# Kernel tuning notes

Hardware: AMD Instinct MI355X
Metric: run time of the kernel (lower is better)

## Reference

```python
import jax, jax.numpy as jnp
import numpy as np

D_MODEL = 1024
NUM_HEADS = 16
D_HEAD = D_MODEL // NUM_HEADS


def setup_inputs() -> dict:
    key = jax.random.key(0)
    ks = jax.random.split(key, 9)
    s = 1.0 / np.sqrt(D_MODEL)
    inp = {"x": jax.random.normal(ks[0], (2, 2048, D_MODEL), dtype=jnp.float32)}
    for i, name in enumerate(["q", "k", "v", "o"]):
        inp[f"W_{name}"] = jax.random.uniform(ks[1 + 2 * i], (D_MODEL, D_MODEL), minval=-s, maxval=s, dtype=jnp.float32)
        inp[f"b_{name}"] = jax.random.uniform(ks[2 + 2 * i], (D_MODEL,), minval=-s, maxval=s, dtype=jnp.float32)
    return inp


def reference(x, W_q, b_q, W_k, b_k, W_v, b_v, W_o, b_o):
    B, S, _ = x.shape
    def heads(W, b):
        # [B,S,D] @ [D,D] -> [B,S,H,Dh] -> [B,H,S,Dh]
        return (x @ W.T + b).reshape(B, S, NUM_HEADS, D_HEAD).transpose(0, 2, 1, 3)
    Q, K, V = heads(W_q, b_q), heads(W_k, b_k), heads(W_v, b_v)
    scores = jnp.einsum("bhqd,bhkd->bhqk", Q, K) / jnp.sqrt(jnp.float32(D_HEAD))
    causal = jnp.tril(jnp.ones((S, S), dtype=bool))  # True = keep
    scores = jnp.where(causal, scores, -jnp.inf)
    A = jax.nn.softmax(scores, axis=-1)
    out = jnp.einsum("bhqk,bhkd->bhqd", A, V)  # [B,H,S,Dh]
    out = out.transpose(0, 2, 1, 3).reshape(B, S, D_MODEL)
    return out @ W_o.T + b_o
```

## Files before the change

### kernel.cpp

```cpp
#include <hip/hip_runtime.h>
#include <math.h>

#define D_MODEL 1024
#define NUM_HEADS 16
#define D_HEAD 64
#define SEQ 2048
#define BATCH 2
#define NROWS (BATCH * SEQ)

typedef short s8v __attribute__((ext_vector_type(8)));
typedef float f4v __attribute__((ext_vector_type(4)));

__device__ __forceinline__ short to_bf(float f) {
    union { float f; unsigned u; } x; x.f = f;
    unsigned r = x.u + 0x7fffu + ((x.u >> 16) & 1u);
    return (short)(r >> 16);
}

__device__ __forceinline__ unsigned pack_bf2(float a, float b) {
    return (unsigned)(unsigned short)to_bf(a) | ((unsigned)(unsigned short)to_bf(b) << 16);
}

__device__ __forceinline__ float fast_exp2(float x) {
    return __builtin_amdgcn_exp2f(x);
}

__device__ __forceinline__ void gld_lds16(const short* g, short* l) {
    __builtin_amdgcn_global_load_lds(
        (const __attribute__((address_space(1))) unsigned*)g,
        (__attribute__((address_space(3))) unsigned*)l, 16, 0, 0);
}

#define QSCALE 0.180336880f

__global__ __launch_bounds__(256) void cvt_fused(
    const float* __restrict__ x,  const float* __restrict__ Wq,
    const float* __restrict__ Wk, const float* __restrict__ Wv,
    const float* __restrict__ Wo,
    short* __restrict__ Xb, short* __restrict__ Wqkvb, short* __restrict__ Wob)
{
    const int NX = NROWS * D_MODEL / 4;
    const int NW = D_MODEL * D_MODEL / 4;
    int j = blockIdx.x * 256 + threadIdx.x;
    const float* src; short* dst; float sc = 1.f;
    if (j < NX)                 { src = x;  dst = Xb; }
    else if ((j -= NX) < NW)    { src = Wq; dst = Wqkvb; sc = QSCALE; }
    else if ((j -= NW) < NW)    { src = Wk; dst = Wqkvb + NW * 4; }
    else if ((j -= NW) < NW)    { src = Wv; dst = Wqkvb + NW * 8; }
    else                        { j -= NW; src = Wo; dst = Wob; }
    float4 v = ((const float4*)src)[j];
    short4 s = { to_bf(v.x * sc), to_bf(v.y * sc), to_bf(v.z * sc), to_bf(v.w * sc) };
    ((short4*)dst)[j] = s;
}

__global__ __launch_bounds__(256) void gemm_qkv(
    const short* __restrict__ Xb, const short* __restrict__ Wb,
    const float* __restrict__ B0, const float* __restrict__ B1, const float* __restrict__ B2,
    short* __restrict__ Q0, short* __restrict__ K1, short* __restrict__ V2)
{
    __shared__ __align__(16) short As[128 * 64];
    __shared__ __align__(16) short Bs[128 * 64];

    const int t    = threadIdx.x;
    const int w    = t >> 6;
    const int lane = t & 63;
    const int quad = lane >> 4;
    const int l15  = lane & 15;
    const int wm   = w & 1, wn = w >> 1;

    const int bx    = blockIdx.x;
    const int xcd   = bx & 7;
    const int g_    = bx >> 3;
    const int n_loc = g_ % 12;
    const int m_loc = g_ / 12;
    const int n0 = ((xcd >> 2) * 12 + n_loc) * 128;
    const int m0 = ((xcd & 3) * 8 + m_loc) * 128;

    const bool swapT = (n0 < 2048);

    f4v acc[4][4];
#pragma unroll
    for (int i = 0; i < 4; ++i)
#pragma unroll
        for (int j = 0; j < 4; ++j) acc[i][j] = (f4v){0.f, 0.f, 0.f, 0.f};

    for (int k0 = 0; k0 < D_MODEL; k0 += 64) {
#pragma unroll
        for (int i = 0; i < 4; ++i) {
            const int cid = i * 256 + t;
            const int row = cid >> 3, kc = cid & 7, g = kc ^ (row & 7);
            gld_lds16(&Xb[(size_t)(m0 + row) * D_MODEL + k0 + g * 8],
                      &As[(i * 256 + w * 64) * 8]);
            gld_lds16(&Wb[(size_t)(n0 + row) * D_MODEL + k0 + g * 8],
                      &Bs[(i * 256 + w * 64) * 8]);
        }
        __syncthreads();

#pragma unroll
        for (int c = 0; c < 2; ++c) {
            s8v af[4], bf[4];
            const int pos = ((c * 4 + quad) ^ (l15 & 7)) * 8;
#pragma unroll
            for (int mi = 0; mi < 4; ++mi)
                af[mi] = *(const s8v*)&As[(wm * 64 + mi * 16 + l15) * 64 + pos];
#pragma unroll
            for (int ni = 0; ni < 4; ++ni)
                bf[ni] = *(const s8v*)&Bs[(wn * 64 + ni * 16 + l15) * 64 + pos];
            if (swapT) {
#pragma unroll
                for (int mi = 0; mi < 4; ++mi)
#pragma unroll
                    for (int ni = 0; ni < 4; ++ni)
                        acc[mi][ni] = __builtin_amdgcn_mfma_f32_16x16x32_bf16(
                            bf[ni], af[mi], acc[mi][ni], 0, 0, 0);
            } else {
#pragma unroll
                for (int mi = 0; mi < 4; ++mi)
#pragma unroll
                    for (int ni = 0; ni < 4; ++ni)
                        acc[mi][ni] = __builtin_amdgcn_mfma_f32_16x16x32_bf16(
                            af[mi], bf[ni], acc[mi][ni], 0, 0, 0);
            }
        }
        __syncthreads();
    }

    if (swapT) {
        const int sel = n0 >> 10;
        const float* bias = sel == 0 ? B0 : B1;
        short* out        = sel == 0 ? Q0 : K1;
        const float bsc   = sel == 0 ? QSCALE : 1.f;
        const int nb = n0 & 1023;
#pragma unroll
        for (int ni = 0; ni < 4; ++ni) {
            const int colb = nb + wn * 64 + ni * 16 + quad * 4;
            float4 bv = *(const float4*)&bias[colb];
            const int h = colb >> 6, dh = colb & 63;
#pragma unroll
            for (int mi = 0; mi < 4; ++mi) {
                const int row = m0 + wm * 64 + mi * 16 + l15;
                const int bb = row >> 11, sl = row & (SEQ - 1);
                int2 pk;
                pk.x = (int)pack_bf2(acc[mi][ni][0] + bv.x * bsc,
                                     acc[mi][ni][1] + bv.y * bsc);
                pk.y = (int)pack_bf2(acc[mi][ni][2] + bv.z * bsc,
                                     acc[mi][ni][3] + bv.w * bsc);
                *(int2*)&out[(((size_t)(bb * NUM_HEADS + h) * SEQ) + sl) * D_HEAD + dh] = pk;
            }
        }
    } else {
        const int nb = n0 & 1023;
#pragma unroll
        for (int ni = 0; ni < 4; ++ni) {
            const int col = nb + wn * 64 + ni * 16 + l15;
            const int h = col >> 6, dh = col & 63;
            const float bv = B2[col];
#pragma unroll
            for (int mi = 0; mi < 4; ++mi) {
                const int row = m0 + wm * 64 + mi * 16 + quad * 4;
                const int bb = row >> 11, sl = row & (SEQ - 1);
                int2 pk;
                pk.x = (int)pack_bf2(acc[mi][ni][0] + bv, acc[mi][ni][1] + bv);
                pk.y = (int)pack_bf2(acc[mi][ni][2] + bv, acc[mi][ni][3] + bv);
                *(int2*)&V2[((size_t)(bb * NUM_HEADS + h) * D_HEAD + dh) * SEQ + sl] = pk;
            }
        }
    }
}

__global__ __launch_bounds__(256) void attn_mfma(
    const short* __restrict__ Qg, const short* __restrict__ Kg,
    const short* __restrict__ Vg,
    short* __restrict__ Op0, short* __restrict__ Op1, float* __restrict__ Lp)
{
    __shared__ __align__(16) short Ps[4][32 * 72];

    const int t    = threadIdx.x;
    const int w    = t >> 6;
    const int lane = t & 63;
    const int quad = lane >> 4;
    const int l15  = lane & 15;

    const int bidx = blockIdx.x;
    const int seg  = bidx >> 9;
    const int p    = bidx & 255;
    const int bh   = p >> 3;
    const int pair = p & 7;
    const int qt   = ((bidx >> 8) & 1) ? 15 - pair : pair;

    const short* qbase = Qg + (size_t)bh * SEQ * D_HEAD;
    const short* kbase = Kg + (size_t)bh * SEQ * D_HEAD;
    const short* vbase = Vg + (size_t)bh * D_HEAD * SEQ;
    const int q0 = qt * 128;
    const int qw = w * 32;

    s8v aq[2][2];
#pragma unroll
    for (int ns = 0; ns < 2; ++ns)
#pragma unroll
        for (int c = 0; c < 2; ++c)
            aq[ns][c] = *(const s8v*)&qbase[(size_t)(q0 + qw + ns * 16 + l15) * D_HEAD
                                            + c * 32 + quad * 8];

    f4v Oacc[2][4];
#pragma unroll
    for (int ms = 0; ms < 2; ++ms)
#pragma unroll
        for (int nt = 0; nt < 4; ++nt) Oacc[ms][nt] = (f4v){0.f, 0.f, 0.f, 0.f};
    float lsum[2] = {0.f, 0.f};

    for (int j = seg; j <= qt; j += 2) {
        const int k0 = j * 128;
        const bool diag = (j == qt);

#pragma unroll
        for (int half = 0; half < 2; ++half) {
            s8v ka[4][2];
#pragma unroll
            for (int mt = 0; mt < 4; ++mt) {
                const int krow = k0 + half * 64 + mt * 16 + l15;
                const short* kr = &kbase[(size_t)krow * D_HEAD + quad * 8];
                ka[mt][0] = *(const s8v*)kr;
                ka[mt][1] = *(const s8v*)(kr + 32);
            }
#pragma unroll
            for (int mt = 0; mt < 4; ++mt) {
#pragma unroll
                for (int ns = 0; ns < 2; ++ns) {
                    f4v st = (f4v){0.f, 0.f, 0.f, 0.f};
                    st = __builtin_amdgcn_mfma_f32_16x16x32_bf16(ka[mt][0], aq[ns][0], st, 0, 0, 0);
                    st = __builtin_amdgcn_mfma_f32_16x16x32_bf16(ka[mt][1], aq[ns][1], st, 0, 0, 0);
                    if (diag) {
#pragma unroll
                        for (int r = 0; r < 4; ++r)
                            if (half * 64 + mt * 16 + quad * 4 + r > qw + ns * 16 + l15)
                                st[r] = -INFINITY;
                    }
                    float e0 = fast_exp2(st[0]), e1 = fast_exp2(st[1]);
                    float e2 = fast_exp2(st[2]), e3 = fast_exp2(st[3]);
                    lsum[ns] += (e0 + e1) + (e2 + e3);
                    int2 pk;
                    pk.x = (int)((__float_as_uint(e0) >> 16) | (__float_as_uint(e1) & 0xffff0000u));
                    pk.y = (int)((__float_as_uint(e2) >> 16) | (__float_as_uint(e3) & 0xffff0000u));
                    *(int2*)&Ps[w][(ns * 16 + l15) * 72 + mt * 16 + quad * 4] = pk;
                }
            }
#pragma unroll
            for (int c2 = 0; c2 < 2; ++c2) {
                s8v ap0 = *(const s8v*)&Ps[w][l15 * 72 + c2 * 32 + quad * 8];
                s8v ap1 = *(const s8v*)&Ps[w][(16 + l15) * 72 + c2 * 32 + quad * 8];
                s8v bv[4];
#pragma unroll
                for (int nt = 0; nt < 4; ++nt)
                    bv[nt] = *(const s8v*)&vbase[(size_t)(nt * 16 + l15) * SEQ
                                                 + k0 + half * 64 + c2 * 32 + quad * 8];
#pragma unroll
                for (int nt = 0; nt < 4; ++nt) {
                    Oacc[0][nt] = __builtin_amdgcn_mfma_f32_16x16x32_bf16(
                        ap0, bv[nt], Oacc[0][nt], 0, 0, 0);
                    Oacc[1][nt] = __builtin_amdgcn_mfma_f32_16x16x32_bf16(
                        ap1, bv[nt], Oacc[1][nt], 0, 0, 0);
                }
            }
        }
    }

#pragma unroll
    for (int ns = 0; ns < 2; ++ns) {
        lsum[ns] += __shfl_xor(lsum[ns], 16, 64);
        lsum[ns] += __shfl_xor(lsum[ns], 32, 64);
    }
    float* L = Lp + ((size_t)seg << 16) + (size_t)bh * SEQ;
    if (quad == 0) {
        L[q0 + qw + l15]      = lsum[0];
        L[q0 + qw + 16 + l15] = lsum[1];
    }
    short* Op = (seg ? Op1 : Op0) + (size_t)bh * SEQ * D_HEAD;
#pragma unroll
    for (int ms = 0; ms < 2; ++ms)
#pragma unroll
        for (int r = 0; r < 4; ++r) {
            const int nloc = q0 + qw + ms * 16 + quad * 4 + r;
            short* dst = Op + (size_t)nloc * D_HEAD + l15;
#pragma unroll
            for (int nt = 0; nt < 4; ++nt)
                dst[nt * 16] = to_bf(Oacc[ms][nt][r]);
        }
}

__global__ __launch_bounds__(256) void gemm_oproj(
    const short* __restrict__ Op0, const short* __restrict__ Op1,
    const float* __restrict__ Lp, const short* __restrict__ Wob,
    const float* __restrict__ bo, float* __restrict__ out)
{
    __shared__ __align__(16) short As[128 * 64];
    __shared__ __align__(16) short Bs[64 * 64];
    __shared__ float invL[NUM_HEADS * 128];

    const int t    = threadIdx.x;
    const int w    = t >> 6;
    const int lane = t & 63;
    const int quad = lane >> 4;
    const int l15  = lane & 15;
    const int wm   = w & 1, wn = w >> 1;

    const int n0 = blockIdx.x * 64;
    const int m0 = blockIdx.y * 128;
    const int bb = m0 >> 11, sloc = m0 & (SEQ - 1);

#pragma unroll
    for (int ii = 0; ii < 8; ++ii) {
        const int idx = t * 8 + ii;
        const int hh = idx >> 7, sl = idx & 127;
        const size_t loff = (size_t)(bb * NUM_HEADS + hh) * SEQ + sloc + sl;
        invL[idx] = 1.f / (Lp[loff] + Lp[65536 + loff]);
    }
    __syncthreads();

    f4v acc[4][2];
#pragma unroll
    for (int i = 0; i < 4; ++i)
#pragma unroll
        for (int j = 0; j < 2; ++j) acc[i][j] = (f4v){0.f, 0.f, 0.f, 0.f};

    for (int k0 = 0; k0 < D_MODEL; k0 += 64) {
        const int h = k0 >> 6;
#pragma unroll
        for (int i = 0; i < 2; ++i) {
            const int cid = i * 256 + w * 64 + lane;
            const int row = cid >> 3, pp = cid & 7, g = pp ^ (row & 7);
            gld_lds16(&Wob[(size_t)(n0 + row) * D_MODEL + k0 + g * 8],
                      &Bs[(i * 256 + w * 64) * 8]);
        }
        const size_t obase = ((size_t)(bb * NUM_HEADS + h) * SEQ + sloc) * D_HEAD;
#pragma unroll
        for (int i = 0; i < 4; ++i) {
            const int cid = i * 256 + t;
            const int row = cid >> 3, pp = cid & 7, g = pp ^ (row & 7);
            const size_t off = obase + (size_t)row * D_HEAD + g * 8;
            int4 a0 = *(const int4*)&Op0[off];
            int4 a1 = *(const int4*)&Op1[off];
            const float inv = invL[h * 128 + row];
            const unsigned* u0 = (const unsigned*)&a0;
            const unsigned* u1 = (const unsigned*)&a1;
            int4 o;
#pragma unroll
            for (int d = 0; d < 4; ++d) {
                float lo = (__uint_as_float(u0[d] << 16) +
                            __uint_as_float(u1[d] << 16)) * inv;
                float hi = (__uint_as_float(u0[d] & 0xffff0000u) +
                            __uint_as_float(u1[d] & 0xffff0000u)) * inv;
                ((unsigned*)&o)[d] = (__float_as_uint(lo) >> 16) |
                                     (__float_as_uint(hi) & 0xffff0000u);
            }
            *(int4*)&As[cid * 8] = o;
        }
        __syncthreads();

#pragma unroll
        for (int c = 0; c < 2; ++c) {
            s8v af[4], bf[2];
            const int pos = ((c * 4 + quad) ^ (l15 & 7)) * 8;
#pragma unroll
            for (int mi = 0; mi < 4; ++mi)
                af[mi] = *(const s8v*)&As[(wm * 64 + mi * 16 + l15) * 64 + pos];
#pragma unroll
            for (int ni = 0; ni < 2; ++ni)
                bf[ni] = *(const s8v*)&Bs[(wn * 32 + ni * 16 + l15) * 64 + pos];
#pragma unroll
            for (int mi = 0; mi < 4; ++mi)
#pragma unroll
                for (int ni = 0; ni < 2; ++ni)
                    acc[mi][ni] = __builtin_amdgcn_mfma_f32_16x16x32_bf16(
                        af[mi], bf[ni], acc[mi][ni], 0, 0, 0);
        }
        __syncthreads();
    }

#pragma unroll
    for (int ni = 0; ni < 2; ++ni) {
        const int col = n0 + wn * 32 + ni * 16 + l15;
        const float bv = bo[col];
#pragma unroll
        for (int mi = 0; mi < 4; ++mi)
#pragma unroll
            for (int r = 0; r < 4; ++r) {
                const int row = m0 + wm * 64 + mi * 16 + quad * 4 + r;
                out[(size_t)row * D_MODEL + col] = acc[mi][ni][r] + bv;
            }
    }
}

extern "C" void kernel_launch(void* const* d_in, const int* in_sizes, int n_in,
                              void* d_out, int out_size, void* d_ws, size_t ws_size,
                              hipStream_t stream)
{
    const float* x  = (const float*)d_in[0];
    const float* Wq = (const float*)d_in[1];
    const float* bq = (const float*)d_in[2];
    const float* Wk = (const float*)d_in[3];
    const float* bk = (const float*)d_in[4];
    const float* Wv = (const float*)d_in[5];
    const float* bv = (const float*)d_in[6];
    const float* Wo = (const float*)d_in[7];
    const float* bo = (const float*)d_in[8];
    float* out = (float*)d_out;

    short* wsp = (short*)d_ws;
    const size_t MAT = (size_t)NROWS * D_MODEL;
    short* Qb    = wsp;
    short* Kbg   = Qb + MAT;
    short* Vtb   = Kbg + MAT;
    short* Xb    = Vtb + 2 * MAT;
    short* Wqkvb = Xb + MAT;
    short* Wob   = Wqkvb + 3 * D_MODEL * D_MODEL;
    short* Op0   = Xb;
    short* Op1   = Wob + D_MODEL * D_MODEL;
    float* Lp    = (float*)(Op1 + MAT);

    cvt_fused<<<8192, 256, 0, stream>>>(x, Wq, Wk, Wv, Wo, Xb, Wqkvb, Wob);

    gemm_qkv<<<768, 256, 0, stream>>>(Xb, Wqkvb, bq, bk, bv, Qb, Kbg, Vtb);

    attn_mfma<<<1024, 256, 0, stream>>>(Qb, Kbg, Vtb, Op0, Op1, Lp);

    gemm_oproj<<<dim3(D_MODEL / 64, NROWS / 128), 256, 0, stream>>>(
        Op0, Op1, Lp, Wob, bo, out);
}
```

Before: 225.8 us.

## Stage K/V tiles in LDS with double-buffered async global-to-LDS loads

Replaces per-warp direct global loads of K and V with block-wide cooperative loads into swizzled, double-buffered LDS tiles of 64 keys. The next tile is prefetched while the current one is computed, and warps skip key halves that are fully masked by causality. This removes 4x redundant global/L2 traffic across warps and overlaps memory with MFMA work. In exchange it adds LDS usage and a block barrier per 64-key step.

```diff
diff --git a/kernel.cpp b/kernel.cpp
--- a/kernel.cpp
+++ b/kernel.cpp
@@ -173,6 +173,8 @@
     const short* __restrict__ Vg,
     short* __restrict__ Op0, short* __restrict__ Op1, float* __restrict__ Lp)
 {
+    __shared__ __align__(16) short Kb[2][64 * 64];
+    __shared__ __align__(16) short Vs[2][64 * 64];
     __shared__ __align__(16) short Ps[4][32 * 72];
 
     const int t    = threadIdx.x;
@@ -209,61 +211,84 @@
         for (int nt = 0; nt < 4; ++nt) Oacc[ms][nt] = (f4v){0.f, 0.f, 0.f, 0.f};
     float lsum[2] = {0.f, 0.f};
 
-    for (int j = seg; j <= qt; j += 2) {
-        const int k0 = j * 128;
-        const bool diag = (j == qt);
-
-#pragma unroll
-        for (int half = 0; half < 2; ++half) {
-            s8v ka[4][2];
-#pragma unroll
-            for (int mt = 0; mt < 4; ++mt) {
-                const int krow = k0 + half * 64 + mt * 16 + l15;
-                const short* kr = &kbase[(size_t)krow * D_HEAD + quad * 8];
-                ka[mt][0] = *(const s8v*)kr;
-                ka[mt][1] = *(const s8v*)(kr + 32);
-            }
-#pragma unroll
-            for (int mt = 0; mt < 4; ++mt) {
-#pragma unroll
-                for (int ns = 0; ns < 2; ++ns) {
-                    f4v st = (f4v){0.f, 0.f, 0.f, 0.f};
-                    st = __builtin_amdgcn_mfma_f32_16x16x32_bf16(ka[mt][0], aq[ns][0], st, 0, 0, 0);
-                    st = __builtin_amdgcn_mfma_f32_16x16x32_bf16(ka[mt][1], aq[ns][1], st, 0, 0, 0);
-                    if (diag) {
-#pragma unroll
-                        for (int r = 0; r < 4; ++r)
-                            if (half * 64 + mt * 16 + quad * 4 + r > qw + ns * 16 + l15)
-                                st[r] = -INFINITY;
-                    }
-                    float e0 = fast_exp2(st[0]), e1 = fast_exp2(st[1]);
-                    float e2 = fast_exp2(st[2]), e3 = fast_exp2(st[3]);
-                    lsum[ns] += (e0 + e1) + (e2 + e3);
-                    int2 pk;
-                    pk.x = (int)((__float_as_uint(e0) >> 16) | (__float_as_uint(e1) & 0xffff0000u));
-                    pk.y = (int)((__float_as_uint(e2) >> 16) | (__float_as_uint(e3) & 0xffff0000u));
-                    *(int2*)&Ps[w][(ns * 16 + l15) * 72 + mt * 16 + quad * 4] = pk;
+    const int niter = (qt >= seg) ? ((((qt - seg) >> 1) + 1) * 2) : 0;
+
+#define STAGE(k0_, b_)                                                          \
+    {                                                                           \
+        const int kk = (k0_);                                                   \
+_Pragma("unroll")                                                               \
+        for (int u = 0; u < 2; ++u) {                                           \
+            const int cid = u * 256 + w * 64 + lane;                            \
+            const int row = cid >> 3, pp = cid & 7, g = pp ^ (row & 7);         \
+            gld_lds16(&kbase[(size_t)(kk + row) * D_HEAD + g * 8],              \
+                      &Kb[b_][(u * 256 + w * 64) * 8]);                         \
+            gld_lds16(&vbase[(size_t)row * SEQ + kk + g * 8],                   \
+                      &Vs[b_][(u * 256 + w * 64) * 8]);                         \
+        }                                                                       \
+    }
+
+    if (niter > 0) STAGE(seg * 128, 0);
+
+    for (int i = 0; i < niter; ++i) {
+        __syncthreads();
+
+        if (i + 1 < niter) {
+            const int i1 = i + 1;
+            const int k1 = (seg + 2 * (i1 >> 1)) * 128 + (i1 & 1) * 64;
+            STAGE(k1, i1 & 1);
+        }
+
+        const int k0   = (seg + 2 * (i >> 1)) * 128 + (i & 1) * 64;
+        const int b    = i & 1;
+        const int koff = k0 - q0;
+        if (koff > qw + 31) continue;
+        const bool diag = (koff + 63 > qw);
+
+#pragma unroll
+        for (int mt = 0; mt < 4; ++mt) {
+            const int krow = mt * 16 + l15;
+            s8v ka0 = *(const s8v*)&Kb[b][(krow * 8 + ((quad) ^ (l15 & 7))) * 8];
+            s8v ka1 = *(const s8v*)&Kb[b][(krow * 8 + ((4 + quad) ^ (l15 & 7))) * 8];
+#pragma unroll
+            for (int ns = 0; ns < 2; ++ns) {
+                f4v st = (f4v){0.f, 0.f, 0.f, 0.f};
+                st = __builtin_amdgcn_mfma_f32_16x16x32_bf16(ka0, aq[ns][0], st, 0, 0, 0);
+                st = __builtin_amdgcn_mfma_f32_16x16x32_bf16(ka1, aq[ns][1], st, 0, 0, 0);
+                if (diag) {
+#pragma unroll
+                    for (int r = 0; r < 4; ++r)
+                        if (koff + mt * 16 + quad * 4 + r > qw + ns * 16 + l15)
+                            st[r] = -INFINITY;
                 }
-            }
-#pragma unroll
-            for (int c2 = 0; c2 < 2; ++c2) {
-                s8v ap0 = *(const s8v*)&Ps[w][l15 * 72 + c2 * 32 + quad * 8];
-                s8v ap1 = *(const s8v*)&Ps[w][(16 + l15) * 72 + c2 * 32 + quad * 8];
-                s8v bv[4];
-#pragma unroll
-                for (int nt = 0; nt < 4; ++nt)
-                    bv[nt] = *(const s8v*)&vbase[(size_t)(nt * 16 + l15) * SEQ
-                                                 + k0 + half * 64 + c2 * 32 + quad * 8];
-#pragma unroll
-                for (int nt = 0; nt < 4; ++nt) {
-                    Oacc[0][nt] = __builtin_amdgcn_mfma_f32_16x16x32_bf16(
-                        ap0, bv[nt], Oacc[0][nt], 0, 0, 0);
-                    Oacc[1][nt] = __builtin_amdgcn_mfma_f32_16x16x32_bf16(
-                        ap1, bv[nt], Oacc[1][nt], 0, 0, 0);
-                }
-            }
-        }
-    }
+                float e0 = fast_exp2(st[0]), e1 = fast_exp2(st[1]);
+                float e2 = fast_exp2(st[2]), e3 = fast_exp2(st[3]);
+                lsum[ns] += (e0 + e1) + (e2 + e3);
+                int2 pk;
+                pk.x = (int)((__float_as_uint(e0) >> 16) | (__float_as_uint(e1) & 0xffff0000u));
+                pk.y = (int)((__float_as_uint(e2) >> 16) | (__float_as_uint(e3) & 0xffff0000u));
+                *(int2*)&Ps[w][(ns * 16 + l15) * 72 + mt * 16 + quad * 4] = pk;
+            }
+        }
+#pragma unroll
+        for (int c2 = 0; c2 < 2; ++c2) {
+            s8v ap0 = *(const s8v*)&Ps[w][l15 * 72 + c2 * 32 + quad * 8];
+            s8v ap1 = *(const s8v*)&Ps[w][(16 + l15) * 72 + c2 * 32 + quad * 8];
+            s8v bv[4];
+#pragma unroll
+            for (int nt = 0; nt < 4; ++nt) {
+                const int vrow = nt * 16 + l15;
+                bv[nt] = *(const s8v*)&Vs[b][(vrow * 8 + ((c2 * 4 + quad) ^ (l15 & 7))) * 8];
+            }
+#pragma unroll
+            for (int nt = 0; nt < 4; ++nt) {
+                Oacc[0][nt] = __builtin_amdgcn_mfma_f32_16x16x32_bf16(
+                    ap0, bv[nt], Oacc[0][nt], 0, 0, 0);
+                Oacc[1][nt] = __builtin_amdgcn_mfma_f32_16x16x32_bf16(
+                    ap1, bv[nt], Oacc[1][nt], 0, 0, 0);
+            }
+        }
+    }
+#undef STAGE
 
 #pragma unroll
     for (int ns = 0; ns < 2; ++ns) {
```

After: 207.3 us. -8.2%, faster.
